# Kernel tuning notes

Measured on AMD Instinct MI355X. Metric: run time of the kernel, lower is better.

## Reference

```python
import jax, jax.numpy as jnp
import numpy as np

HIDDEN = 1024
HEADS = 16
HEAD_DIM = HIDDEN // HEADS
MAX_SEQ = 2048
BATCH = 2
SEQ = 2048


def setup_inputs() -> dict:
    key = jax.random.key(0)
    ks = jax.random.split(key, 6)
    x = jax.random.normal(ks[0], (BATCH, SEQ, HIDDEN), dtype=jnp.float32)
    # torch Linear params expressed as [in, out] weight + bias
    W1 = jax.random.normal(ks[1], (HIDDEN, 4 * HIDDEN), dtype=jnp.float32) * (HIDDEN ** -0.5)
    b1 = jnp.zeros((4 * HIDDEN,), dtype=jnp.float32)
    W2 = jax.random.normal(ks[2], (HIDDEN, HIDDEN), dtype=jnp.float32) * (HIDDEN ** -0.5)
    b2 = jnp.zeros((HIDDEN,), dtype=jnp.float32)
    rel_table = jax.random.normal(ks[3], (2 * MAX_SEQ - 1, HEADS), dtype=jnp.float32) * 0.02
    # causal mask [B, S, S]; True = keep
    attn_mask = jnp.broadcast_to(jnp.tril(jnp.ones((SEQ, SEQ), dtype=bool)), (BATCH, SEQ, SEQ))
    return {"x": x, "W1": W1, "b1": b1, "W2": W2, "b2": b2,
            "rel_table": rel_table, "attn_mask": attn_mask}


def reference(x, W1, b1, W2, b2, rel_table, attn_mask):
    B, S, H = x.shape
    # fused projection + SiLU, then chunk into U, Q, K, V
    activated = jax.nn.silu(jnp.einsum('bsh,hf->bsf', x, W1) + b1)
    U, Qp, Kp, Vp = jnp.split(activated, 4, axis=-1)
    # [B, nH, S, hd]
    def heads(t):
        return t.reshape(B, S, HEADS, HEAD_DIM).transpose(0, 2, 1, 3)
    Q, K, V = heads(Qp), heads(Kp), heads(Vp)
    scale = HEAD_DIM ** -0.5
    scores = jnp.einsum('bnqd,bnkd->bnqk', Q, K) * scale
    # relative position bias gather: idx[i,j] = i - j + MAX_SEQ - 1
    pos = jnp.arange(S)
    rel_idx = pos[:, None] - pos[None, :] + (MAX_SEQ - 1)  # [S, S]
    rel_bias = rel_table[rel_idx].transpose(2, 0, 1)[None]  # [1, nH, S, S]
    scores = scores + rel_bias
    attn = jax.nn.silu(scores)
    attn = jnp.where(attn_mask[:, None, :, :], attn, 0.0)
    out = jnp.einsum('bnqk,bnkd->bnqd', attn, V)
    out = out.transpose(0, 2, 1, 3).reshape(B, S, H)
    gated = out * U
    return jnp.einsum('bsh,hf->bsf', gated, W2) + b2
```

## Files before the change

kernel.cpp:

```cpp
#include <hip/hip_runtime.h>
#include <math.h>

#define HIDDEN   1024
#define HEADS    16
#define HEAD_DIM 64
#define SEQ      2048
#define BATCH    2
#define FDIM     4096
#define MTOT     4096
#define MAXSEQ   2048

typedef __bf16 bf16x8 __attribute__((ext_vector_type(8)));
typedef float  f32x4  __attribute__((ext_vector_type(4)));
typedef unsigned short u16;

__device__ __forceinline__ float silu_f(float v) {
    return v / (1.f + __expf(-v));
}

__device__ __forceinline__ u16 f2bf(float f) {
    union { float f; unsigned u; } v; v.f = f;
    unsigned r = v.u + 0x7FFFu + ((v.u >> 16) & 1u);
    return (u16)(r >> 16);
}
__device__ __forceinline__ float bf2f(u16 b) {
    union { unsigned u; float f; } v; v.u = ((unsigned)b) << 16;
    return v.f;
}

__device__ __forceinline__ void gload16(const void* g, void* l) {
    __builtin_amdgcn_global_load_lds(
        (const __attribute__((address_space(1))) void*)g,
        (__attribute__((address_space(3))) void*)l, 16, 0, 0);
}

__global__ __launch_bounds__(256) void convert_x_kernel(
    const float* __restrict__ src, u16* __restrict__ dst)
{
    int idx = (blockIdx.x * 256 + threadIdx.x) * 8;
    float4 a = *(const float4*)&src[idx];
    float4 b = *(const float4*)&src[idx + 4];
    u16 h8[8] = {f2bf(a.x), f2bf(a.y), f2bf(a.z), f2bf(a.w),
                 f2bf(b.x), f2bf(b.y), f2bf(b.z), f2bf(b.w)};
    *(float4*)&dst[idx] = *(float4*)h8;
}

__global__ __launch_bounds__(256) void transpose_convert_kernel(
    const float* __restrict__ W, u16* __restrict__ Wt, int rows, int cols)
{
    __shared__ u16 T[64][72];
    const int tid = threadIdx.x;
    const int r0 = blockIdx.y * 64, c0 = blockIdx.x * 64;
#pragma unroll
    for (int l = 0; l < 4; ++l) {
        int idx = tid + l * 256;
        int row = idx >> 4;
        int c4  = (idx & 15) * 4;
        float4 v = *(const float4*)&W[(size_t)(r0 + row) * cols + c0 + c4];
        T[c4 + 0][row] = f2bf(v.x);
        T[c4 + 1][row] = f2bf(v.y);
        T[c4 + 2][row] = f2bf(v.z);
        T[c4 + 3][row] = f2bf(v.w);
    }
    __syncthreads();
#pragma unroll
    for (int l = 0; l < 2; ++l) {
        int idx = tid + l * 256;
        int row = idx >> 3;
        int cb  = (idx & 7) * 8;
        *(float4*)&Wt[(size_t)(c0 + row) * rows + r0 + cb] = *(float4*)&T[row][cb];
    }
}

#define GEMM_CORE(A_PTR, BT_PTR, KDIM)                                         \
    __shared__ __align__(16) u16 As[128 * 64];                                 \
    __shared__ __align__(16) u16 Bs[128 * 64];                                 \
    const int tid  = threadIdx.x;                                              \
    const int lane = tid & 63;                                                 \
    const int w    = tid >> 6;                                                 \
    const int wm   = w & 1, wn = w >> 1;                                       \
    const int l16  = lane & 15, quad = lane >> 4;                              \
    const int m0   = blockIdx.y * 128;                                         \
    const int n0   = blockIdx.x * 128;                                         \
    const int srow = lane >> 3;                                                \
    const int scol = (lane & 7) * 8;                                           \
    f32x4 acc[4][4];                                                           \
    _Pragma("unroll")                                                          \
    for (int mt = 0; mt < 4; ++mt)                                             \
        _Pragma("unroll")                                                      \
        for (int nt = 0; nt < 4; ++nt)                                         \
            acc[mt][nt] = (f32x4){0.f, 0.f, 0.f, 0.f};                         \
    for (int k0 = 0; k0 < (KDIM); k0 += 64) {                                  \
        __syncthreads();                                                       \
        _Pragma("unroll")                                                      \
        for (int i = 0; i < 4; ++i) {                                          \
            int ci  = w * 4 + i;                                               \
            int row = ci * 8 + srow;                                           \
            unsigned off = __builtin_amdgcn_readfirstlane(ci * 1024);          \
            gload16(&(A_PTR)[(size_t)(m0 + row) * (KDIM) + k0 + scol],         \
                    (char*)As + off);                                          \
            gload16(&(BT_PTR)[(size_t)(n0 + row) * (KDIM) + k0 + scol],        \
                    (char*)Bs + off);                                          \
        }                                                                      \
        __syncthreads();                                                       \
        _Pragma("unroll")                                                      \
        for (int kc = 0; kc < 2; ++kc) {                                       \
            bf16x8 af[4], bfr[4];                                              \
            _Pragma("unroll")                                                  \
            for (int t = 0; t < 4; ++t) {                                      \
                af[t]  = *(const bf16x8*)&As[(wm * 64 + t * 16 + l16) * 64 +   \
                                             kc * 32 + quad * 8];              \
                bfr[t] = *(const bf16x8*)&Bs[(wn * 64 + t * 16 + l16) * 64 +   \
                                             kc * 32 + quad * 8];              \
            }                                                                  \
            _Pragma("unroll")                                                  \
            for (int mt = 0; mt < 4; ++mt)                                     \
                _Pragma("unroll")                                              \
                for (int nt = 0; nt < 4; ++nt)                                 \
                    acc[mt][nt] = __builtin_amdgcn_mfma_f32_16x16x32_bf16(     \
                        af[mt], bfr[nt], acc[mt][nt], 0, 0, 0);                \
        }                                                                      \
    }

__global__ __launch_bounds__(256) void gemm1_mfma_kernel(
    const u16* __restrict__ A, const u16* __restrict__ Bt,
    const float* __restrict__ b1,
    u16* __restrict__ Ub, u16* __restrict__ Qh,
    u16* __restrict__ Kh, u16* __restrict__ Vh)
{
    GEMM_CORE(A, Bt, HIDDEN)

    const int chunk = n0 >> 10;
    float bias[4]; int nloc[4];
#pragma unroll
    for (int nt = 0; nt < 4; ++nt) {
        int n = n0 + wn * 64 + nt * 16 + l16;
        bias[nt] = b1[n];
        nloc[nt] = n & 1023;
    }
    u16* dstbase = (chunk == 0) ? Ub : (chunk == 1) ? Qh : (chunk == 2) ? Kh : Vh;
#pragma unroll
    for (int mt = 0; mt < 4; ++mt) {
#pragma unroll
        for (int r = 0; r < 4; ++r) {
            int m  = m0 + wm * 64 + mt * 16 + quad * 4 + r;
            int bb = m >> 11, s = m & 2047;
#pragma unroll
            for (int nt = 0; nt < 4; ++nt) {
                float v = silu_f(acc[mt][nt][r] + bias[nt]);
                size_t o;
                if (chunk == 0) {
                    o = (size_t)m * 1024 + nloc[nt];
                } else {
                    int h = nloc[nt] >> 6, d = nloc[nt] & 63;
                    o = (size_t)(((bb * HEADS + h) * SEQ) + s) * HEAD_DIM + d;
                }
                dstbase[o] = f2bf(v);
            }
        }
    }
}

__global__ __launch_bounds__(256) void gemm2_mfma_kernel(
    const u16* __restrict__ A, const u16* __restrict__ Bt,
    const float* __restrict__ b2, float* __restrict__ Out)
{
    GEMM_CORE(A, Bt, HIDDEN)

    float bias[4]; int ncol[4];
#pragma unroll
    for (int nt = 0; nt < 4; ++nt) {
        int n = n0 + wn * 64 + nt * 16 + l16;
        bias[nt] = b2[n];
        ncol[nt] = n;
    }
#pragma unroll
    for (int mt = 0; mt < 4; ++mt) {
#pragma unroll
        for (int r = 0; r < 4; ++r) {
            int m = m0 + wm * 64 + mt * 16 + quad * 4 + r;
#pragma unroll
            for (int nt = 0; nt < 4; ++nt)
                Out[(size_t)m * 1024 + ncol[nt]] = acc[mt][nt][r] + bias[nt];
        }
    }
}

#define PS 72

__global__ __launch_bounds__(256) void attn_mfma_kernel(
    const u16* __restrict__ Qh, const u16* __restrict__ Kh,
    const u16* __restrict__ Vh, const float* __restrict__ rel,
    const u16* __restrict__ Ub, u16* __restrict__ G)
{
    __shared__ u16 Qs[64][PS];
    __shared__ u16 Ks[2][64][PS];
    __shared__ u16 Vt[2][64][PS];
    __shared__ u16 Ps[64][PS];
    __shared__ float rel_sh[2112];

    const int tid  = threadIdx.x;
    const int lane = tid & 63;
    const int w    = tid >> 6;
    const int quad = lane >> 4;
    const int l16  = lane & 15;
    const int h    = blockIdx.y;
    const int bb   = blockIdx.z;

    const u16* Kg = Kh + (size_t)((bb * HEADS + h) * SEQ) * HEAD_DIM;
    const u16* Vg = Vh + (size_t)((bb * HEADS + h) * SEQ) * HEAD_DIM;

    for (int i = tid; i < 2111; i += 256)
        rel_sh[i] = rel[(size_t)(1984 + i) * HEADS + h];

    const int k_r  = tid >> 3;
    const int k_c  = (tid & 7) * 8;
    const int v_k  = (tid & 31) * 2;
    const int v_d  = (tid >> 5) * 8;

    for (int half = 0; half < 2; ++half) {
        const int qt = half ? (31 - (int)blockIdx.x) : (int)blockIdx.x;
        const int q0 = qt * 64;
        const u16* Qg = Qh + (size_t)((bb * HEADS + h) * SEQ + q0) * HEAD_DIM;

        __syncthreads();

#pragma unroll
        for (int l = 0; l < 2; ++l) {
            int idx = tid + l * 256;
            int row = idx >> 3, cb = (idx & 7) * 8;
            *(float4*)&Qs[row][cb] = *(const float4*)&Qg[row * HEAD_DIM + cb];
        }

        float4 kreg0, kreg1, vreg0, vreg1;
        kreg0 = *(const float4*)&Kg[(size_t)(0 + k_r) * HEAD_DIM + k_c];
        kreg1 = *(const float4*)&Kg[(size_t)(0 + k_r + 32) * HEAD_DIM + k_c];
        vreg0 = *(const float4*)&Vg[(size_t)(0 + v_k) * HEAD_DIM + v_d];
        vreg1 = *(const float4*)&Vg[(size_t)(0 + v_k + 1) * HEAD_DIM + v_d];

        f32x4 o[4];
#pragma unroll
        for (int dt = 0; dt < 4; ++dt) o[dt] = (f32x4){0.f, 0.f, 0.f, 0.f};

        for (int kt = 0; kt <= qt; ++kt) {
            const int k0 = kt * 64;
            const int b  = kt & 1;

            *(float4*)&Ks[b][k_r][k_c]      = kreg0;
            *(float4*)&Ks[b][k_r + 32][k_c] = kreg1;
            {
                union { float4 f; u16 u[8]; } a0, a1;
                a0.f = vreg0; a1.f = vreg1;
#pragma unroll
                for (int i = 0; i < 8; ++i) {
                    unsigned pv = (unsigned)a0.u[i] | ((unsigned)a1.u[i] << 16);
                    *(unsigned*)&Vt[b][v_d + i][v_k] = pv;
                }
            }
            __syncthreads();

            if (kt < qt) {
                const int kn = k0 + 64;
                kreg0 = *(const float4*)&Kg[(size_t)(kn + k_r) * HEAD_DIM + k_c];
                kreg1 = *(const float4*)&Kg[(size_t)(kn + k_r + 32) * HEAD_DIM + k_c];
                vreg0 = *(const float4*)&Vg[(size_t)(kn + v_k) * HEAD_DIM + v_d];
                vreg1 = *(const float4*)&Vg[(size_t)(kn + v_k + 1) * HEAD_DIM + v_d];
            }

            bf16x8 qa0 = *(const bf16x8*)&Qs[w * 16 + l16][quad * 8];
            bf16x8 qa1 = *(const bf16x8*)&Qs[w * 16 + l16][32 + quad * 8];

            const int qrel = q0 + w * 16 + l16 - k0;

#pragma unroll
            for (int ct = 0; ct < 4; ++ct) {
                bf16x8 ka0 = *(const bf16x8*)&Ks[b][ct * 16 + l16][quad * 8];
                bf16x8 ka1 = *(const bf16x8*)&Ks[b][ct * 16 + l16][32 + quad * 8];
                f32x4 sc = {0.f, 0.f, 0.f, 0.f};
                sc = __builtin_amdgcn_mfma_f32_16x16x32_bf16(ka0, qa0, sc, 0, 0, 0);
                sc = __builtin_amdgcn_mfma_f32_16x16x32_bf16(ka1, qa1, sc, 0, 0, 0);
                u16 pk[4];
#pragma unroll
                for (int r = 0; r < 4; ++r) {
                    int kloc = ct * 16 + quad * 4 + r;
                    int dloc = qrel - kloc;
                    float s  = sc[r] * 0.125f + rel_sh[dloc + 63];
                    float p  = (dloc >= 0) ? silu_f(s) : 0.f;
                    pk[r] = f2bf(p);
                }
                *(uint2*)&Ps[w * 16 + l16][ct * 16 + quad * 4] = *(uint2*)pk;
            }

            bf16x8 pa0 = *(const bf16x8*)&Ps[w * 16 + l16][quad * 8];
            bf16x8 pa1 = *(const bf16x8*)&Ps[w * 16 + l16][32 + quad * 8];
#pragma unroll
            for (int dt = 0; dt < 4; ++dt) {
                bf16x8 vb0 = *(const bf16x8*)&Vt[b][dt * 16 + l16][quad * 8];
                bf16x8 vb1 = *(const bf16x8*)&Vt[b][dt * 16 + l16][32 + quad * 8];
                o[dt] = __builtin_amdgcn_mfma_f32_16x16x32_bf16(pa0, vb0, o[dt], 0, 0, 0);
                o[dt] = __builtin_amdgcn_mfma_f32_16x16x32_bf16(pa1, vb1, o[dt], 0, 0, 0);
            }
        }

#pragma unroll
        for (int dt = 0; dt < 4; ++dt)
#pragma unroll
            for (int r = 0; r < 4; ++r) {
                int q = q0 + w * 16 + quad * 4 + r;
                size_t base = (size_t)(bb * SEQ + q) * HIDDEN +
                              h * HEAD_DIM + dt * 16 + l16;
                float u = bf2f(Ub[base]);
                G[base] = f2bf(o[dt][r] * u);
            }
    }
}

extern "C" void kernel_launch(void* const* d_in, const int* in_sizes, int n_in,
                              void* d_out, int out_size, void* d_ws, size_t ws_size,
                              hipStream_t stream)
{
    const float* X   = (const float*)d_in[0];
    const float* W1  = (const float*)d_in[1];
    const float* b1  = (const float*)d_in[2];
    const float* W2  = (const float*)d_in[3];
    const float* b2  = (const float*)d_in[4];
    const float* rel = (const float*)d_in[5];
    float* out = (float*)d_out;

    const size_t MH = (size_t)MTOT * HIDDEN;
    u16* Ub  = (u16*)d_ws;
    u16* Qh  = Ub  + MH;
    u16* Kh  = Qh  + MH;
    u16* Vh  = Kh  + MH;
    u16* G   = Vh  + MH;
    u16* Xb  = G   + MH;
    u16* W1t = Xb  + MH;
    u16* W2t = W1t + MH;

    convert_x_kernel<<<MTOT * HIDDEN / 2048, 256, 0, stream>>>(X, Xb);
    transpose_convert_kernel<<<dim3(FDIM / 64, HIDDEN / 64), 256, 0, stream>>>(
        W1, W1t, HIDDEN, FDIM);
    transpose_convert_kernel<<<dim3(HIDDEN / 64, HIDDEN / 64), 256, 0, stream>>>(
        W2, W2t, HIDDEN, HIDDEN);
    gemm1_mfma_kernel<<<dim3(FDIM / 128, MTOT / 128), 256, 0, stream>>>(
        Xb, W1t, b1, Ub, Qh, Kh, Vh);
    attn_mfma_kernel<<<dim3(16, HEADS, BATCH), 256, 0, stream>>>(
        Qh, Kh, Vh, rel, Ub, G);
    gemm2_mfma_kernel<<<dim3(HIDDEN / 128, MTOT / 128), 256, 0, stream>>>(
        G, W2t, b2, out);
}
```

Before: 280.8 us.

## Split attention into one block per query tile with smaller LDS footprint

The attention kernel now launches one block per (batch, head, query tile) instead of pairing two tiles per block. Q moves from shared memory into registers, K/V use a single buffer, and the relative-bias slice is streamed per key tile, which shrinks shared memory and targets higher occupancy (launch bounds 256,4). The 1/8 score scale is folded into Q in the GEMM1 epilogue, SiLU uses a reciprocal intrinsic, and P is packed with a paired bf16 conversion. The single buffer needs an extra barrier per iteration, and the causal work is no longer balanced inside each block.

```diff
diff --git a/kernel.cpp b/kernel.cpp
--- a/kernel.cpp
+++ b/kernel.cpp
@@ -1,4 +1,5 @@
 #include <hip/hip_runtime.h>
+#include <hip/hip_bf16.h>
 #include <math.h>
 
 #define HIDDEN   1024
@@ -14,8 +15,8 @@
 typedef float  f32x4  __attribute__((ext_vector_type(4)));
 typedef unsigned short u16;
 
-__device__ __forceinline__ float silu_f(float v) {
-    return v / (1.f + __expf(-v));
+__device__ __forceinline__ float silu_fast(float v) {
+    return v * __builtin_amdgcn_rcpf(1.f + __expf(-v));
 }
 
 __device__ __forceinline__ u16 f2bf(float f) {
@@ -26,6 +27,11 @@
 __device__ __forceinline__ float bf2f(u16 b) {
     union { unsigned u; float f; } v; v.u = ((unsigned)b) << 16;
     return v.f;
+}
+__device__ __forceinline__ unsigned pk2(float a, float b) {
+    union { __hip_bfloat162 h; unsigned u; } z;
+    z.h = __float22bfloat162_rn(make_float2(a, b));
+    return z.u;
 }
 
 __device__ __forceinline__ void gload16(const void* g, void* l) {
@@ -139,6 +145,7 @@
         nloc[nt] = n & 1023;
     }
     u16* dstbase = (chunk == 0) ? Ub : (chunk == 1) ? Qh : (chunk == 2) ? Kh : Vh;
+    const float postscale = (chunk == 1) ? 0.125f : 1.0f;
 #pragma unroll
     for (int mt = 0; mt < 4; ++mt) {
 #pragma unroll
@@ -147,7 +154,7 @@
             int bb = m >> 11, s = m & 2047;
 #pragma unroll
             for (int nt = 0; nt < 4; ++nt) {
-                float v = silu_f(acc[mt][nt][r] + bias[nt]);
+                float v = silu_fast(acc[mt][nt][r] + bias[nt]) * postscale;
                 size_t o;
                 if (chunk == 0) {
                     o = (size_t)m * 1024 + nloc[nt];
@@ -188,131 +195,118 @@
 
 #define PS 72
 
-__global__ __launch_bounds__(256) void attn_mfma_kernel(
+__global__ __launch_bounds__(256, 4) void attn_mfma_kernel(
     const u16* __restrict__ Qh, const u16* __restrict__ Kh,
     const u16* __restrict__ Vh, const float* __restrict__ rel,
     const u16* __restrict__ Ub, u16* __restrict__ G)
 {
-    __shared__ u16 Qs[64][PS];
-    __shared__ u16 Ks[2][64][PS];
-    __shared__ u16 Vt[2][64][PS];
+    __shared__ u16 Ks[64][PS];
+    __shared__ u16 Vt[64][PS];
     __shared__ u16 Ps[64][PS];
-    __shared__ float rel_sh[2112];
+    __shared__ float rel_sh[128];
 
     const int tid  = threadIdx.x;
     const int lane = tid & 63;
     const int w    = tid >> 6;
     const int quad = lane >> 4;
     const int l16  = lane & 15;
-    const int h    = blockIdx.y;
-    const int bb   = blockIdx.z;
+
+    const int bid   = blockIdx.x;
+    const int x5    = bid & 31;
+    const int h     = (bid >> 5) & 15;
+    const int bb    = bid >> 9;
+    const int phase = (bid >> 8) & 1;
+    const int qt    = phase ? (31 - x5) : x5;
+    const int q0    = qt * 64;
 
     const u16* Kg = Kh + (size_t)((bb * HEADS + h) * SEQ) * HEAD_DIM;
     const u16* Vg = Vh + (size_t)((bb * HEADS + h) * SEQ) * HEAD_DIM;
-
-    for (int i = tid; i < 2111; i += 256)
-        rel_sh[i] = rel[(size_t)(1984 + i) * HEADS + h];
-
-    const int k_r  = tid >> 3;
-    const int k_c  = (tid & 7) * 8;
-    const int v_k  = (tid & 31) * 2;
-    const int v_d  = (tid >> 5) * 8;
-
-    for (int half = 0; half < 2; ++half) {
-        const int qt = half ? (31 - (int)blockIdx.x) : (int)blockIdx.x;
-        const int q0 = qt * 64;
-        const u16* Qg = Qh + (size_t)((bb * HEADS + h) * SEQ + q0) * HEAD_DIM;
-
+    const u16* Qg = Qh + (size_t)((bb * HEADS + h) * SEQ + q0) * HEAD_DIM;
+
+    const int qrow = w * 16 + l16;
+    bf16x8 qa0 = *(const bf16x8*)&Qg[qrow * HEAD_DIM + quad * 8];
+    bf16x8 qa1 = *(const bf16x8*)&Qg[qrow * HEAD_DIM + 32 + quad * 8];
+
+    const int k_r = tid >> 3,      k_c = (tid & 7) * 8;
+    const int v_k = (tid & 31) * 2, v_d = (tid >> 5) * 8;
+
+    float4 kreg0 = *(const float4*)&Kg[(size_t)k_r * HEAD_DIM + k_c];
+    float4 kreg1 = *(const float4*)&Kg[(size_t)(k_r + 32) * HEAD_DIM + k_c];
+    float4 vreg0 = *(const float4*)&Vg[(size_t)v_k * HEAD_DIM + v_d];
+    float4 vreg1 = *(const float4*)&Vg[(size_t)(v_k + 1) * HEAD_DIM + v_d];
+    float  relreg = 0.f;
+    if (tid < 127) relreg = rel[(size_t)(q0 + 1984 + tid) * HEADS + h];
+
+    f32x4 o[4];
+#pragma unroll
+    for (int dt = 0; dt < 4; ++dt) o[dt] = (f32x4){0.f, 0.f, 0.f, 0.f};
+
+    for (int kt = 0; kt <= qt; ++kt) {
+        *(float4*)&Ks[k_r][k_c]      = kreg0;
+        *(float4*)&Ks[k_r + 32][k_c] = kreg1;
+        {
+            union { float4 f; u16 u[8]; } a0, a1;
+            a0.f = vreg0; a1.f = vreg1;
+#pragma unroll
+            for (int i = 0; i < 8; ++i)
+                *(unsigned*)&Vt[v_d + i][v_k] =
+                    (unsigned)a0.u[i] | ((unsigned)a1.u[i] << 16);
+        }
+        if (tid < 127) rel_sh[tid] = relreg;
         __syncthreads();
 
-#pragma unroll
-        for (int l = 0; l < 2; ++l) {
-            int idx = tid + l * 256;
-            int row = idx >> 3, cb = (idx & 7) * 8;
-            *(float4*)&Qs[row][cb] = *(const float4*)&Qg[row * HEAD_DIM + cb];
-        }
-
-        float4 kreg0, kreg1, vreg0, vreg1;
-        kreg0 = *(const float4*)&Kg[(size_t)(0 + k_r) * HEAD_DIM + k_c];
-        kreg1 = *(const float4*)&Kg[(size_t)(0 + k_r + 32) * HEAD_DIM + k_c];
-        vreg0 = *(const float4*)&Vg[(size_t)(0 + v_k) * HEAD_DIM + v_d];
-        vreg1 = *(const float4*)&Vg[(size_t)(0 + v_k + 1) * HEAD_DIM + v_d];
-
-        f32x4 o[4];
-#pragma unroll
-        for (int dt = 0; dt < 4; ++dt) o[dt] = (f32x4){0.f, 0.f, 0.f, 0.f};
-
-        for (int kt = 0; kt <= qt; ++kt) {
-            const int k0 = kt * 64;
-            const int b  = kt & 1;
-
-            *(float4*)&Ks[b][k_r][k_c]      = kreg0;
-            *(float4*)&Ks[b][k_r + 32][k_c] = kreg1;
-            {
-                union { float4 f; u16 u[8]; } a0, a1;
-                a0.f = vreg0; a1.f = vreg1;
-#pragma unroll
-                for (int i = 0; i < 8; ++i) {
-                    unsigned pv = (unsigned)a0.u[i] | ((unsigned)a1.u[i] << 16);
-                    *(unsigned*)&Vt[b][v_d + i][v_k] = pv;
-                }
+        if (kt < qt) {
+            const int kn = (kt + 1) * 64;
+            kreg0 = *(const float4*)&Kg[(size_t)(kn + k_r) * HEAD_DIM + k_c];
+            kreg1 = *(const float4*)&Kg[(size_t)(kn + k_r + 32) * HEAD_DIM + k_c];
+            vreg0 = *(const float4*)&Vg[(size_t)(kn + v_k) * HEAD_DIM + v_d];
+            vreg1 = *(const float4*)&Vg[(size_t)(kn + v_k + 1) * HEAD_DIM + v_d];
+            if (tid < 127)
+                relreg = rel[(size_t)(q0 - kn + 1984 + tid) * HEADS + h];
+        }
+
+        const int qrel = q0 - kt * 64 + qrow;
+
+#pragma unroll
+        for (int ct = 0; ct < 4; ++ct) {
+            bf16x8 ka0 = *(const bf16x8*)&Ks[ct * 16 + l16][quad * 8];
+            bf16x8 ka1 = *(const bf16x8*)&Ks[ct * 16 + l16][32 + quad * 8];
+            f32x4 sc = {0.f, 0.f, 0.f, 0.f};
+            sc = __builtin_amdgcn_mfma_f32_16x16x32_bf16(ka0, qa0, sc, 0, 0, 0);
+            sc = __builtin_amdgcn_mfma_f32_16x16x32_bf16(ka1, qa1, sc, 0, 0, 0);
+            float p[4];
+#pragma unroll
+            for (int r = 0; r < 4; ++r) {
+                int kloc = ct * 16 + quad * 4 + r;
+                float s  = sc[r] + rel_sh[qrow - kloc + 63];
+                p[r] = (qrel - kloc >= 0) ? silu_fast(s) : 0.f;
             }
-            __syncthreads();
-
-            if (kt < qt) {
-                const int kn = k0 + 64;
-                kreg0 = *(const float4*)&Kg[(size_t)(kn + k_r) * HEAD_DIM + k_c];
-                kreg1 = *(const float4*)&Kg[(size_t)(kn + k_r + 32) * HEAD_DIM + k_c];
-                vreg0 = *(const float4*)&Vg[(size_t)(kn + v_k) * HEAD_DIM + v_d];
-                vreg1 = *(const float4*)&Vg[(size_t)(kn + v_k + 1) * HEAD_DIM + v_d];
-            }
-
-            bf16x8 qa0 = *(const bf16x8*)&Qs[w * 16 + l16][quad * 8];
-            bf16x8 qa1 = *(const bf16x8*)&Qs[w * 16 + l16][32 + quad * 8];
-
-            const int qrel = q0 + w * 16 + l16 - k0;
-
-#pragma unroll
-            for (int ct = 0; ct < 4; ++ct) {
-                bf16x8 ka0 = *(const bf16x8*)&Ks[b][ct * 16 + l16][quad * 8];
-                bf16x8 ka1 = *(const bf16x8*)&Ks[b][ct * 16 + l16][32 + quad * 8];
-                f32x4 sc = {0.f, 0.f, 0.f, 0.f};
-                sc = __builtin_amdgcn_mfma_f32_16x16x32_bf16(ka0, qa0, sc, 0, 0, 0);
-                sc = __builtin_amdgcn_mfma_f32_16x16x32_bf16(ka1, qa1, sc, 0, 0, 0);
-                u16 pk[4];
-#pragma unroll
-                for (int r = 0; r < 4; ++r) {
-                    int kloc = ct * 16 + quad * 4 + r;
-                    int dloc = qrel - kloc;
-                    float s  = sc[r] * 0.125f + rel_sh[dloc + 63];
-                    float p  = (dloc >= 0) ? silu_f(s) : 0.f;
-                    pk[r] = f2bf(p);
-                }
-                *(uint2*)&Ps[w * 16 + l16][ct * 16 + quad * 4] = *(uint2*)pk;
-            }
-
-            bf16x8 pa0 = *(const bf16x8*)&Ps[w * 16 + l16][quad * 8];
-            bf16x8 pa1 = *(const bf16x8*)&Ps[w * 16 + l16][32 + quad * 8];
-#pragma unroll
-            for (int dt = 0; dt < 4; ++dt) {
-                bf16x8 vb0 = *(const bf16x8*)&Vt[b][dt * 16 + l16][quad * 8];
-                bf16x8 vb1 = *(const bf16x8*)&Vt[b][dt * 16 + l16][32 + quad * 8];
-                o[dt] = __builtin_amdgcn_mfma_f32_16x16x32_bf16(pa0, vb0, o[dt], 0, 0, 0);
-                o[dt] = __builtin_amdgcn_mfma_f32_16x16x32_bf16(pa1, vb1, o[dt], 0, 0, 0);
-            }
-        }
-
-#pragma unroll
-        for (int dt = 0; dt < 4; ++dt)
-#pragma unroll
-            for (int r = 0; r < 4; ++r) {
-                int q = q0 + w * 16 + quad * 4 + r;
-                size_t base = (size_t)(bb * SEQ + q) * HIDDEN +
-                              h * HEAD_DIM + dt * 16 + l16;
-                float u = bf2f(Ub[base]);
-                G[base] = f2bf(o[dt][r] * u);
-            }
-    }
+            uint2 pk = make_uint2(pk2(p[0], p[1]), pk2(p[2], p[3]));
+            *(uint2*)&Ps[qrow][ct * 16 + quad * 4] = pk;
+        }
+
+        bf16x8 pa0 = *(const bf16x8*)&Ps[qrow][quad * 8];
+        bf16x8 pa1 = *(const bf16x8*)&Ps[qrow][32 + quad * 8];
+#pragma unroll
+        for (int dt = 0; dt < 4; ++dt) {
+            bf16x8 vb0 = *(const bf16x8*)&Vt[dt * 16 + l16][quad * 8];
+            bf16x8 vb1 = *(const bf16x8*)&Vt[dt * 16 + l16][32 + quad * 8];
+            o[dt] = __builtin_amdgcn_mfma_f32_16x16x32_bf16(pa0, vb0, o[dt], 0, 0, 0);
+            o[dt] = __builtin_amdgcn_mfma_f32_16x16x32_bf16(pa1, vb1, o[dt], 0, 0, 0);
+        }
+        __syncthreads();
+    }
+
+#pragma unroll
+    for (int dt = 0; dt < 4; ++dt)
+#pragma unroll
+        for (int r = 0; r < 4; ++r) {
+            int q = q0 + w * 16 + quad * 4 + r;
+            size_t base = (size_t)(bb * SEQ + q) * HIDDEN +
+                          h * HEAD_DIM + dt * 16 + l16;
+            float u = bf2f(Ub[base]);
+            G[base] = f2bf(o[dt][r] * u);
+        }
 }
 
 extern "C" void kernel_launch(void* const* d_in, const int* in_sizes, int n_in,
@@ -344,7 +338,7 @@
         W2, W2t, HIDDEN, HIDDEN);
     gemm1_mfma_kernel<<<dim3(FDIM / 128, MTOT / 128), 256, 0, stream>>>(
         Xb, W1t, b1, Ub, Qh, Kh, Vh);
-    attn_mfma_kernel<<<dim3(16, HEADS, BATCH), 256, 0, stream>>>(
+    attn_mfma_kernel<<<dim3(1024), 256, 0, stream>>>(
         Qh, Kh, Vh, rel, Ub, G);
     gemm2_mfma_kernel<<<dim3(HIDDEN / 128, MTOT / 128), 256, 0, stream>>>(
         G, W2t, b2, out);
```

New measurement: 259.4 us. 1.08x faster.
